# Kernel optimization log

Measured on AMD Instinct MI355X. Metric: run time of the kernel, lower is better.

## Reference

```python
import jax, jax.numpy as jnp
import numpy as np

DIM_Q = 512
DIM_K = 512
DIM_V = 512
NUM_HEADS = 8
B, NQ, NK = 4, 2048, 2048


def _linear_init(key, d_in, d_out):
    kw, kb = jax.random.split(key)
    bound = 1.0 / np.sqrt(d_in)
    W = jax.random.uniform(kw, (d_in, d_out), minval=-bound, maxval=bound, dtype=jnp.float32)
    b = jax.random.uniform(kb, (d_out,), minval=-bound, maxval=bound, dtype=jnp.float32)
    return W, b


def setup_inputs() -> dict:
    key = jax.random.key(0)
    ks = jax.random.split(key, 6)
    Q = jax.random.normal(ks[0], (B, NQ, DIM_Q), dtype=jnp.float32)
    K = jax.random.normal(ks[1], (B, NK, DIM_K), dtype=jnp.float32)
    Wq, bq = _linear_init(ks[2], DIM_Q, DIM_V)
    Wk, bk = _linear_init(ks[3], DIM_K, DIM_V)
    Wv, bv = _linear_init(ks[4], DIM_K, DIM_V)
    Wo, bo = _linear_init(ks[5], DIM_V, DIM_V)
    ln0_g = jnp.ones((DIM_V,), jnp.float32)
    ln0_b = jnp.zeros((DIM_V,), jnp.float32)
    ln1_g = jnp.ones((DIM_V,), jnp.float32)
    ln1_b = jnp.zeros((DIM_V,), jnp.float32)
    return {"Q": Q, "K": K, "Wq": Wq, "bq": bq, "Wk": Wk, "bk": bk,
            "Wv": Wv, "bv": bv, "Wo": Wo, "bo": bo,
            "ln0_g": ln0_g, "ln0_b": ln0_b, "ln1_g": ln1_g, "ln1_b": ln1_b}


def _layer_norm(x, g, b, eps=1e-5):
    mu = jnp.mean(x, axis=-1, keepdims=True)
    var = jnp.mean(jnp.square(x - mu), axis=-1, keepdims=True)
    return (x - mu) * jax.lax.rsqrt(var + eps) * g + b


def reference(Q, K, Wq, bq, Wk, bk, Wv, bv, Wo, bo, ln0_g, ln0_b, ln1_g, ln1_b):
    h = NUM_HEADS
    dh = DIM_V // h
    q = Q @ Wq + bq                      # [B, NQ, DIM_V]
    k = K @ Wk + bk                      # [B, NK, DIM_V]
    v = K @ Wv + bv                      # [B, NK, DIM_V]
    qh = q.reshape(B, NQ, h, dh)
    kh = k.reshape(B, NK, h, dh)
    vh = v.reshape(B, NK, h, dh)
    # NOTE: faithful to original — scale by sqrt(dim_V), not sqrt(head_dim)
    scores = jnp.einsum('bqhd,bkhd->bhqk', qh, kh) / jnp.sqrt(jnp.float32(DIM_V))
    A = jax.nn.softmax(scores, axis=-1)  # [B, h, NQ, NK]
    o = jnp.einsum('bhqk,bkhd->bqhd', A, vh) + qh
    H = o.reshape(B, NQ, DIM_V)          # residual with projected Q
    H = _layer_norm(H, ln0_g, ln0_b)
    H = H + jax.nn.relu(H @ Wo + bo)
    H = _layer_norm(H, ln1_g, ln1_b)
    return H
```

## Files before the change

kernel.cpp:

```cpp
#include <hip/hip_runtime.h>

typedef float f32x4 __attribute__((ext_vector_type(4)));
typedef __bf16 bf16x8 __attribute__((ext_vector_type(8)));
typedef unsigned short u16;
typedef u16 u16x8 __attribute__((ext_vector_type(8)));
typedef u16 u16x4 __attribute__((ext_vector_type(4)));

#define SCALE2F (0.044194173824159216f * 1.4426950408889634f)
#define UNSCALE (1.0f / SCALE2F)

__device__ __forceinline__ u16 f2bf(float x){ return __builtin_bit_cast(u16, (__bf16)x); }
__device__ __forceinline__ float bf2f(u16 h){ unsigned u = ((unsigned)h) << 16; return __builtin_bit_cast(float, u); }
__device__ __forceinline__ int swz(int r, int byteInRow){ return (r*128 + byteInRow) ^ ((r & 7) << 4); }
__device__ __forceinline__ void gload16(const void* g, void* l) {
  __builtin_amdgcn_global_load_lds(
      (const __attribute__((address_space(1))) void*)g,
      (__attribute__((address_space(3))) void*)l, 16, 0, 0);
}

#define MFMA(a,b,c) __builtin_amdgcn_mfma_f32_16x16x32_bf16((a),(b),(c),0,0,0)

__global__ __launch_bounds__(256) void wprep_k(
    const float* __restrict__ W0, const float* __restrict__ W1,
    const float* __restrict__ W2, const float* __restrict__ W3,
    u16* __restrict__ wt)
{
  __shared__ float tile[64][68];
  const float* Ws[4] = {W0, W1, W2, W3};
  const float* W = Ws[blockIdx.z];
  const float sc = (blockIdx.z == 0) ? SCALE2F : 1.0f;
  u16* out = wt + (size_t)blockIdx.z * 512 * 512;
  int k0 = blockIdx.x * 64, n0 = blockIdx.y * 64;
  int t = threadIdx.x;
  #pragma unroll
  for (int i = 0; i < 2; ++i) {
    int c = t + i*256; int r = c >> 3, k8 = c & 7;
    const float* src = W + (size_t)(k0 + r)*512 + n0 + k8*8;
    *(f32x4*)&tile[r][k8*8]     = *(const f32x4*)src;
    *(f32x4*)&tile[r][k8*8 + 4] = *(const f32x4*)(src + 4);
  }
  __syncthreads();
  #pragma unroll
  for (int i = 0; i < 2; ++i) {
    int c = t + i*256; int r = c >> 3, k8 = c & 7;
    u16x8 h;
    #pragma unroll
    for (int j = 0; j < 8; ++j) h[j] = f2bf(tile[k8*8 + j][r] * sc);
    *(u16x8*)(out + (size_t)(n0 + r)*512 + k0 + k8*8) = h;
  }
}

__global__ __launch_bounds__(512) void proj3_k(
    const float* __restrict__ Qin, const float* __restrict__ Kin,
    const u16* __restrict__ wt,
    const float* __restrict__ bq, const float* __restrict__ bk, const float* __restrict__ bv,
    u16* __restrict__ qbuf, u16* __restrict__ kbuf, u16* __restrict__ vt)
{
  __shared__ __align__(16) u16 lA[2][64*64];
  __shared__ __align__(16) u16 lB[2][128*64];
  int z = blockIdx.z;
  const float* A    = (z == 0) ? Qin : Kin;
  const u16*   Bt   = wt + (size_t)z * 262144;
  const float* bias = (z == 0) ? bq : (z == 1) ? bk : bv;
  const float bscale = (z == 0) ? SCALE2F : 1.0f;
  int row0 = blockIdx.x * 64, col0 = blockIdx.y * 128;
  int t = threadIdx.x, lane = t & 63, wid = t >> 6;
  int wr = wid >> 2, wc = wid & 3;
  int l15 = lane & 15, lg = lane >> 4;
  int ar = t >> 3, ak8 = t & 7;
  int br = t >> 3;
  int bsrc = (((t & 7) << 4) ^ ((br & 7) << 4)) >> 1;
  const float* Arow = A + (size_t)row0 * 512;
  const u16*   Brow = Bt + (size_t)col0 * 512;

  f32x4 acc[2][2] = {};

  #pragma unroll
  for (int i = 0; i < 2; ++i)
    gload16(Brow + (size_t)(br + i*64)*512 + bsrc, (char*)lB[0] + i*8192 + t*16);
  {
    const float* src = Arow + (size_t)ar*512 + ak8*8;
    f32x4 x0 = *(const f32x4*)src;
    f32x4 x1 = *(const f32x4*)(src + 4);
    u16x8 h;
    #pragma unroll
    for (int j = 0; j < 4; ++j) { h[j] = f2bf(x0[j]); h[j+4] = f2bf(x1[j]); }
    *(u16x8*)((char*)lA[0] + swz(ar, ak8*16)) = h;
  }
  __syncthreads();

  int cur = 0;
  for (int k0 = 0; k0 < 512; k0 += 64) {
    bool pf = (k0 + 64 < 512);
    f32x4 px0, px1;
    if (pf) {
      #pragma unroll
      for (int i = 0; i < 2; ++i)
        gload16(Brow + (size_t)(br + i*64)*512 + k0 + 64 + bsrc, (char*)lB[cur^1] + i*8192 + t*16);
      const float* src = Arow + (size_t)ar*512 + k0 + 64 + ak8*8;
      px0 = *(const f32x4*)src;
      px1 = *(const f32x4*)(src + 4);
    }
    const char* lAc = (const char*)lA[cur];
    const char* lBc = (const char*)lB[cur];
    #pragma unroll
    for (int ks = 0; ks < 2; ++ks) {
      bf16x8 af[2], bfv[2];
      #pragma unroll
      for (int m = 0; m < 2; ++m)
        af[m] = *(const bf16x8*)(lAc + swz(wr*32 + m*16 + l15, ks*64 + lg*16));
      #pragma unroll
      for (int n = 0; n < 2; ++n)
        bfv[n] = *(const bf16x8*)(lBc + swz(wc*32 + n*16 + l15, ks*64 + lg*16));
      #pragma unroll
      for (int m = 0; m < 2; ++m)
        #pragma unroll
        for (int n = 0; n < 2; ++n)
          acc[m][n] = MFMA(af[m], bfv[n], acc[m][n]);
    }
    if (pf) {
      u16x8 h;
      #pragma unroll
      for (int j = 0; j < 4; ++j) { h[j] = f2bf(px0[j]); h[j+4] = f2bf(px1[j]); }
      *(u16x8*)((char*)lA[cur^1] + swz(ar, ak8*16)) = h;
    }
    __syncthreads();
    cur ^= 1;
  }

  if (z < 2) {
    u16* out = z ? kbuf : qbuf;
    #pragma unroll
    for (int m = 0; m < 2; ++m) {
      int rowg = row0 + wr*32 + m*16 + lg*4;
      #pragma unroll
      for (int n = 0; n < 2; ++n) {
        int colg = col0 + wc*32 + n*16 + l15;
        float bvv = bias[colg] * bscale;
        #pragma unroll
        for (int r = 0; r < 4; ++r)
          out[(size_t)(rowg + r)*512 + colg] = f2bf(acc[m][n][r] + bvv);
      }
    }
  } else {
    #pragma unroll
    for (int m = 0; m < 2; ++m) {
      int rowg = row0 + wr*32 + m*16 + lg*4;
      int b = rowg >> 11, ntok = rowg & 2047;
      #pragma unroll
      for (int n = 0; n < 2; ++n) {
        int colg = col0 + wc*32 + n*16 + l15;
        float bvv = bias[colg];
        u16x4 hv;
        #pragma unroll
        for (int r = 0; r < 4; ++r) hv[r] = f2bf(acc[m][n][r] + bvv);
        *(u16x4*)(vt + ((size_t)b*512 + colg)*2048 + ntok) = hv;
      }
    }
  }
}

__global__ __launch_bounds__(512) void gemmo_k(
    const u16* __restrict__ A, const u16* __restrict__ Bt,
    const float* __restrict__ bias, float* __restrict__ outf,
    const u16* __restrict__ resid)
{
  __shared__ __align__(16) u16 lA[2][64*64];
  __shared__ __align__(16) u16 lB[2][128*64];
  int row0 = blockIdx.x * 64, col0 = blockIdx.y * 128;
  int t = threadIdx.x, lane = t & 63, wid = t >> 6;
  int wr = wid >> 2, wc = wid & 3;
  int l15 = lane & 15, lg = lane >> 4;
  int ar = t >> 3;
  int asrc = (((t & 7) << 4) ^ ((ar & 7) << 4)) >> 1;
  const u16* Arow = A + (size_t)row0 * 512;
  const u16* Brow = Bt + (size_t)col0 * 512;
  f32x4 acc[2][2] = {};

  gload16(Arow + (size_t)ar*512 + asrc, (char*)lA[0] + t*16);
  #pragma unroll
  for (int i = 0; i < 2; ++i)
    gload16(Brow + (size_t)(ar + i*64)*512 + asrc, (char*)lB[0] + i*8192 + t*16);
  __syncthreads();

  int cur = 0;
  for (int k0 = 0; k0 < 512; k0 += 64) {
    if (k0 + 64 < 512) {
      gload16(Arow + (size_t)ar*512 + k0 + 64 + asrc, (char*)lA[cur^1] + t*16);
      #pragma unroll
      for (int i = 0; i < 2; ++i)
        gload16(Brow + (size_t)(ar + i*64)*512 + k0 + 64 + asrc, (char*)lB[cur^1] + i*8192 + t*16);
    }
    const char* lAc = (const char*)lA[cur];
    const char* lBc = (const char*)lB[cur];
    #pragma unroll
    for (int ks = 0; ks < 2; ++ks) {
      bf16x8 af[2], bfv[2];
      #pragma unroll
      for (int m = 0; m < 2; ++m)
        af[m] = *(const bf16x8*)(lAc + swz(wr*32 + m*16 + l15, ks*64 + lg*16));
      #pragma unroll
      for (int n = 0; n < 2; ++n)
        bfv[n] = *(const bf16x8*)(lBc + swz(wc*32 + n*16 + l15, ks*64 + lg*16));
      #pragma unroll
      for (int m = 0; m < 2; ++m)
        #pragma unroll
        for (int n = 0; n < 2; ++n)
          acc[m][n] = MFMA(af[m], bfv[n], acc[m][n]);
    }
    __syncthreads();
    cur ^= 1;
  }
  #pragma unroll
  for (int m = 0; m < 2; ++m) {
    int rowg = row0 + wr*32 + m*16 + lg*4;
    #pragma unroll
    for (int n = 0; n < 2; ++n) {
      int colg = col0 + wc*32 + n*16 + l15;
      float bvv = bias[colg];
      #pragma unroll
      for (int r = 0; r < 4; ++r) {
        size_t idx = (size_t)(rowg + r)*512 + colg;
        outf[idx] = bf2f(resid[idx]) + fmaxf(acc[m][n][r] + bvv, 0.0f);
      }
    }
  }
}

__global__ __launch_bounds__(512) void attn_k(
    const u16* __restrict__ qb, const u16* __restrict__ kb,
    const u16* __restrict__ vt, float* __restrict__ opart, float* __restrict__ psb)
{
  __shared__ __align__(16) u16 lK[2][64*64];
  __shared__ __align__(16) u16 lV[2][64*64];
  __shared__ __align__(16) u16 pl[8][16][72];

  int t = threadIdx.x, lane = t & 63, wid = t >> 6;
  int bh = blockIdx.y;
  int b = bh >> 3, h = bh & 7;
  int zkv = blockIdx.z;
  int kvbeg = zkv * 1024, kvend = kvbeg + 1024;
  int q0 = blockIdx.x * 128 + wid * 16;
  int l15 = lane & 15, lg = lane >> 4;

  const u16* kbase = kb + ((size_t)b*2048)*512 + h*64;
  const u16* vbase = vt + ((size_t)b*512 + h*64)*2048;

  int sr = t >> 3;
  int ssrc = (((t & 7) << 4) ^ ((sr & 7) << 4)) >> 1;

  bf16x8 aq[2];
  {
    const u16* qp = qb + ((size_t)(b*2048 + q0 + l15))*512 + h*64 + lg*8;
    aq[0] = *(const bf16x8*)qp;
    aq[1] = *(const bf16x8*)(qp + 32);
  }

  f32x4 acco[4] = {};
  float ps = 0.0f;

  gload16(kbase + (size_t)(kvbeg + sr)*512 + ssrc, (char*)lK[0] + t*16);
  gload16(vbase + (size_t)sr*2048 + kvbeg + ssrc, (char*)lV[0] + t*16);
  __syncthreads();

  int cur = 0;
  for (int t0 = kvbeg; t0 < kvend; t0 += 64) {
    if (t0 + 64 < kvend) {
      gload16(kbase + (size_t)(t0 + 64 + sr)*512 + ssrc, (char*)lK[cur^1] + t*16);
      gload16(vbase + (size_t)sr*2048 + t0 + 64 + ssrc, (char*)lV[cur^1] + t*16);
    }
    f32x4 s[4] = {};
    const char* lKc = (const char*)lK[cur];
    #pragma unroll
    for (int n = 0; n < 4; ++n) {
      int row = n*16 + l15;
      bf16x8 bk0 = *(const bf16x8*)(lKc + swz(row, lg*16));
      bf16x8 bk1 = *(const bf16x8*)(lKc + swz(row, 64 + lg*16));
      s[n] = MFMA(bk0, aq[0], s[n]);
      s[n] = MFMA(bk1, aq[1], s[n]);
    }
    #pragma unroll
    for (int n = 0; n < 4; ++n) {
      u16x4 hp;
      #pragma unroll
      for (int r = 0; r < 4; ++r) {
        float p = __builtin_amdgcn_exp2f(s[n][r]);
        ps += p;
        hp[r] = f2bf(p);
      }
      *(u16x4*)&pl[wid][l15][n*16 + lg*4] = hp;
    }
    const char* lVc = (const char*)lV[cur];
    #pragma unroll
    for (int ks = 0; ks < 2; ++ks) {
      bf16x8 pb = *(const bf16x8*)&pl[wid][l15][ks*32 + lg*8];
      #pragma unroll
      for (int n = 0; n < 4; ++n) {
        bf16x8 av = *(const bf16x8*)(lVc + swz(n*16 + l15, ks*64 + lg*16));
        acco[n] = MFMA(av, pb, acco[n]);
      }
    }
    __syncthreads();
    cur ^= 1;
  }
  ps += __shfl_xor(ps, 16, 64);
  ps += __shfl_xor(ps, 32, 64);
  float* obase = opart + (((size_t)zkv*4 + b)*2048 + q0 + l15)*512 + h*64;
  #pragma unroll
  for (int n = 0; n < 4; ++n)
    *(f32x4*)(obase + n*16 + lg*4) = acco[n];
  if (lg == 0)
    psb[((size_t)zkv*32 + bh)*2048 + q0 + l15] = ps;
}

__global__ __launch_bounds__(256) void ln0c_k(
    const float* __restrict__ opart, const float* __restrict__ psb,
    const u16* __restrict__ qb, const float* __restrict__ gam,
    const float* __restrict__ bet, u16* __restrict__ yh)
{
  int t = threadIdx.x, lane = t & 63, w = t >> 6;
  size_t row = (size_t)blockIdx.x * 4 + w;
  int b = (int)(row >> 11), q = (int)(row & 2047);
  int head = lane >> 3;
  float sa = psb[((size_t)b*8 + head)*2048 + q] +
             psb[((size_t)32 + b*8 + head)*2048 + q];
  float inv = 1.0f / sa;
  const float* xa = opart + row*512 + lane*8;
  const float* xb = xa + (size_t)8192*512;
  f32x4 a0 = *(const f32x4*)xa,      a1 = *(const f32x4*)(xa + 4);
  f32x4 b0v = *(const f32x4*)xb,     b1v = *(const f32x4*)(xb + 4);
  u16x8 qr = *(const u16x8*)(qb + row*512 + lane*8);
  f32x4 v0, v1;
  #pragma unroll
  for (int j = 0; j < 4; ++j) {
    v0[j] = (a0[j] + b0v[j])*inv + bf2f(qr[j])*UNSCALE;
    v1[j] = (a1[j] + b1v[j])*inv + bf2f(qr[j+4])*UNSCALE;
  }
  float s = 0.0f, ss = 0.0f;
  #pragma unroll
  for (int j = 0; j < 4; ++j) {
    s += v0[j] + v1[j];
    ss += v0[j]*v0[j] + v1[j]*v1[j];
  }
  #pragma unroll
  for (int m = 1; m < 64; m <<= 1) { s += __shfl_xor(s, m, 64); ss += __shfl_xor(ss, m, 64); }
  float mu = s * (1.0f/512.0f);
  float var = ss * (1.0f/512.0f) - mu*mu;
  float rs = rsqrtf(var + 1e-5f);
  const float* gp = gam + lane*8;
  const float* bp = bet + lane*8;
  f32x4 g0 = *(const f32x4*)gp, g1 = *(const f32x4*)(gp + 4);
  f32x4 be0 = *(const f32x4*)bp, be1 = *(const f32x4*)(bp + 4);
  u16x8 hv;
  #pragma unroll
  for (int j = 0; j < 4; ++j) {
    hv[j]   = f2bf((v0[j] - mu)*rs*g0[j] + be0[j]);
    hv[j+4] = f2bf((v1[j] - mu)*rs*g1[j] + be1[j]);
  }
  *(u16x8*)(yh + row*512 + lane*8) = hv;
}

__global__ __launch_bounds__(256) void ln_k(
    const float* __restrict__ x, const float* __restrict__ gam,
    const float* __restrict__ bet, float* __restrict__ y)
{
  int t = threadIdx.x, lane = t & 63, w = t >> 6;
  size_t row = (size_t)blockIdx.x * 4 + w;
  const float* xp = x + row*512 + lane*8;
  f32x4 v0 = *(const f32x4*)xp;
  f32x4 v1 = *(const f32x4*)(xp + 4);
  float s = 0.0f, ss = 0.0f;
  #pragma unroll
  for (int j = 0; j < 4; ++j) {
    s += v0[j] + v1[j];
    ss += v0[j]*v0[j] + v1[j]*v1[j];
  }
  #pragma unroll
  for (int m = 1; m < 64; m <<= 1) { s += __shfl_xor(s, m, 64); ss += __shfl_xor(ss, m, 64); }
  float mu = s * (1.0f/512.0f);
  float var = ss * (1.0f/512.0f) - mu*mu;
  float rs = rsqrtf(var + 1e-5f);
  const float* gp = gam + lane*8;
  const float* bp = bet + lane*8;
  f32x4 g0 = *(const f32x4*)gp, g1 = *(const f32x4*)(gp + 4);
  f32x4 b0 = *(const f32x4*)bp, b1 = *(const f32x4*)(bp + 4);
  f32x4 o0, o1;
  #pragma unroll
  for (int j = 0; j < 4; ++j) {
    o0[j] = (v0[j] - mu)*rs*g0[j] + b0[j];
    o1[j] = (v1[j] - mu)*rs*g1[j] + b1[j];
  }
  float* yp = y + row*512 + lane*8;
  *(f32x4*)yp = o0;
  *(f32x4*)(yp + 4) = o1;
}

extern "C" void kernel_launch(void* const* d_in, const int* in_sizes, int n_in,
                              void* d_out, int out_size, void* d_ws, size_t ws_size,
                              hipStream_t stream)
{
  const float* Q   = (const float*)d_in[0];
  const float* K   = (const float*)d_in[1];
  const float* Wq  = (const float*)d_in[2];
  const float* bq  = (const float*)d_in[3];
  const float* Wk  = (const float*)d_in[4];
  const float* bk  = (const float*)d_in[5];
  const float* Wv  = (const float*)d_in[6];
  const float* bv  = (const float*)d_in[7];
  const float* Wo  = (const float*)d_in[8];
  const float* bo  = (const float*)d_in[9];
  const float* g0  = (const float*)d_in[10];
  const float* b0  = (const float*)d_in[11];
  const float* g1  = (const float*)d_in[12];
  const float* b1  = (const float*)d_in[13];

  char* ws = (char*)d_ws;
  u16*   wt    = (u16*)(ws + 0);
  u16*   qbuf  = (u16*)(ws + (2u<<20));
  u16*   kbuf  = (u16*)(ws + (10u<<20));
  u16*   vt    = (u16*)(ws + (18u<<20));
  float* opart = (float*)(ws + (26u<<20));
  float* psb   = (float*)(ws + (58u<<20));
  u16*   Hbuf  = (u16*)(ws + (10u<<20));
  float* Gbuf  = (float*)(ws + (26u<<20));

  wprep_k<<<dim3(8, 8, 4), 256, 0, stream>>>(Wq, Wk, Wv, Wo, wt);
  proj3_k<<<dim3(128, 4, 3), 512, 0, stream>>>(Q, K, wt, bq, bk, bv, qbuf, kbuf, vt);
  attn_k<<<dim3(16, 32, 2), 512, 0, stream>>>(qbuf, kbuf, vt, opart, psb);
  ln0c_k<<<2048, 256, 0, stream>>>(opart, psb, qbuf, g0, b0, Hbuf);
  gemmo_k<<<dim3(128, 4), 512, 0, stream>>>(Hbuf, wt + 3*262144, bo, Gbuf, Hbuf);
  ln_k<<<2048, 256, 0, stream>>>(Gbuf, g1, b1, (float*)d_out);
}
```

Before: 113.6 us.

## Use 32x32x16 MFMA in attention with 32 query rows per wave

The attention kernel moves from 16x16x32 to 32x32x16 bf16 MFMA, so each wave handles 32 query rows instead of 16 and each block covers 256 queries, halving the grid in x. Each K/V tile loaded into LDS is therefore reused across twice as many queries, cutting K/V global and LDS traffic per query and the number of MFMA instructions issued. The cost is more accumulator registers (two 16-float accumulators plus a 16-float score tile) and a larger per-wave P staging buffer. The grid falls to 512 blocks, which may underfill the GPU, and launch_bounds now requests 4 blocks per CU.

```diff
diff --git a/kernel.cpp b/kernel.cpp
--- a/kernel.cpp
+++ b/kernel.cpp
@@ -1,6 +1,7 @@
 #include <hip/hip_runtime.h>
 
 typedef float f32x4 __attribute__((ext_vector_type(4)));
+typedef float f32x16 __attribute__((ext_vector_type(16)));
 typedef __bf16 bf16x8 __attribute__((ext_vector_type(8)));
 typedef unsigned short u16;
 typedef u16 u16x8 __attribute__((ext_vector_type(8)));
@@ -18,7 +19,8 @@
       (__attribute__((address_space(3))) void*)l, 16, 0, 0);
 }
 
-#define MFMA(a,b,c) __builtin_amdgcn_mfma_f32_16x16x32_bf16((a),(b),(c),0,0,0)
+#define MFMA(a,b,c)   __builtin_amdgcn_mfma_f32_16x16x32_bf16((a),(b),(c),0,0,0)
+#define MFMA32(a,b,c) __builtin_amdgcn_mfma_f32_32x32x16_bf16((a),(b),(c),0,0,0)
 
 __global__ __launch_bounds__(256) void wprep_k(
     const float* __restrict__ W0, const float* __restrict__ W1,
@@ -227,21 +229,21 @@
   }
 }
 
-__global__ __launch_bounds__(512) void attn_k(
+__global__ __launch_bounds__(512, 4) void attn_k(
     const u16* __restrict__ qb, const u16* __restrict__ kb,
     const u16* __restrict__ vt, float* __restrict__ opart, float* __restrict__ psb)
 {
   __shared__ __align__(16) u16 lK[2][64*64];
   __shared__ __align__(16) u16 lV[2][64*64];
-  __shared__ __align__(16) u16 pl[8][16][72];
+  __shared__ __align__(16) u16 pl[8][32][72];
 
   int t = threadIdx.x, lane = t & 63, wid = t >> 6;
   int bh = blockIdx.y;
   int b = bh >> 3, h = bh & 7;
   int zkv = blockIdx.z;
   int kvbeg = zkv * 1024, kvend = kvbeg + 1024;
-  int q0 = blockIdx.x * 128 + wid * 16;
-  int l15 = lane & 15, lg = lane >> 4;
+  int q0 = blockIdx.x * 256 + wid * 32;
+  int l31 = lane & 31, hi = lane >> 5;
 
   const u16* kbase = kb + ((size_t)b*2048)*512 + h*64;
   const u16* vbase = vt + ((size_t)b*512 + h*64)*2048;
@@ -249,14 +251,14 @@
   int sr = t >> 3;
   int ssrc = (((t & 7) << 4) ^ ((sr & 7) << 4)) >> 1;
 
-  bf16x8 aq[2];
+  bf16x8 aq[4];
   {
-    const u16* qp = qb + ((size_t)(b*2048 + q0 + l15))*512 + h*64 + lg*8;
-    aq[0] = *(const bf16x8*)qp;
-    aq[1] = *(const bf16x8*)(qp + 32);
-  }
-
-  f32x4 acco[4] = {};
+    const u16* qp = qb + ((size_t)(b*2048 + q0 + l31))*512 + h*64 + hi*8;
+    #pragma unroll
+    for (int ks = 0; ks < 4; ++ks) aq[ks] = *(const bf16x8*)(qp + ks*16);
+  }
+
+  f32x16 acco[2] = {};
   float ps = 0.0f;
 
   gload16(kbase + (size_t)(kvbeg + sr)*512 + ssrc, (char*)lK[0] + t*16);
@@ -269,48 +271,55 @@
       gload16(kbase + (size_t)(t0 + 64 + sr)*512 + ssrc, (char*)lK[cur^1] + t*16);
       gload16(vbase + (size_t)sr*2048 + t0 + 64 + ssrc, (char*)lV[cur^1] + t*16);
     }
-    f32x4 s[4] = {};
     const char* lKc = (const char*)lK[cur];
-    #pragma unroll
-    for (int n = 0; n < 4; ++n) {
-      int row = n*16 + l15;
-      bf16x8 bk0 = *(const bf16x8*)(lKc + swz(row, lg*16));
-      bf16x8 bk1 = *(const bf16x8*)(lKc + swz(row, 64 + lg*16));
-      s[n] = MFMA(bk0, aq[0], s[n]);
-      s[n] = MFMA(bk1, aq[1], s[n]);
-    }
-    #pragma unroll
-    for (int n = 0; n < 4; ++n) {
-      u16x4 hp;
-      #pragma unroll
-      for (int r = 0; r < 4; ++r) {
-        float p = __builtin_amdgcn_exp2f(s[n][r]);
-        ps += p;
-        hp[r] = f2bf(p);
-      }
-      *(u16x4*)&pl[wid][l15][n*16 + lg*4] = hp;
-    }
     const char* lVc = (const char*)lV[cur];
     #pragma unroll
-    for (int ks = 0; ks < 2; ++ks) {
-      bf16x8 pb = *(const bf16x8*)&pl[wid][l15][ks*32 + lg*8];
-      #pragma unroll
-      for (int n = 0; n < 4; ++n) {
-        bf16x8 av = *(const bf16x8*)(lVc + swz(n*16 + l15, ks*64 + lg*16));
-        acco[n] = MFMA(av, pb, acco[n]);
-      }
-    }
+    for (int n = 0; n < 2; ++n) {
+      f32x16 s = {};
+      #pragma unroll
+      for (int ks = 0; ks < 4; ++ks) {
+        bf16x8 kf = *(const bf16x8*)(lKc + swz(n*32 + l31, ks*32 + hi*16));
+        s = MFMA32(kf, aq[ks], s);
+      }
+      #pragma unroll
+      for (int rq = 0; rq < 4; ++rq) {
+        u16x4 hp;
+        #pragma unroll
+        for (int e = 0; e < 4; ++e) {
+          float p = __builtin_amdgcn_exp2f(s[rq*4 + e]);
+          ps += p;
+          hp[e] = f2bf(p);
+        }
+        *(u16x4*)&pl[wid][l31][n*32 + rq*8 + hi*4] = hp;
+      }
+    }
+    bf16x8 pf[4];
+    #pragma unroll
+    for (int ks = 0; ks < 4; ++ks)
+      pf[ks] = *(const bf16x8*)&pl[wid][l31][ks*16 + hi*8];
+    #pragma unroll
+    for (int m = 0; m < 2; ++m)
+      #pragma unroll
+      for (int ks = 0; ks < 4; ++ks) {
+        bf16x8 vf = *(const bf16x8*)(lVc + swz(m*32 + l31, ks*32 + hi*16));
+        acco[m] = MFMA32(vf, pf[ks], acco[m]);
+      }
     __syncthreads();
     cur ^= 1;
   }
-  ps += __shfl_xor(ps, 16, 64);
   ps += __shfl_xor(ps, 32, 64);
-  float* obase = opart + (((size_t)zkv*4 + b)*2048 + q0 + l15)*512 + h*64;
-  #pragma unroll
-  for (int n = 0; n < 4; ++n)
-    *(f32x4*)(obase + n*16 + lg*4) = acco[n];
-  if (lg == 0)
-    psb[((size_t)zkv*32 + bh)*2048 + q0 + l15] = ps;
+  float* obase = opart + (((size_t)zkv*4 + b)*2048 + q0 + l31)*512 + h*64;
+  #pragma unroll
+  for (int m = 0; m < 2; ++m)
+    #pragma unroll
+    for (int rq = 0; rq < 4; ++rq) {
+      f32x4 ov;
+      #pragma unroll
+      for (int e = 0; e < 4; ++e) ov[e] = acco[m][rq*4 + e];
+      *(f32x4*)(obase + m*32 + rq*8 + hi*4) = ov;
+    }
+  if (hi == 0)
+    psb[((size_t)zkv*32 + bh)*2048 + q0 + l31] = ps;
 }
 
 __global__ __launch_bounds__(256) void ln0c_k(
@@ -426,7 +435,7 @@
 
   wprep_k<<<dim3(8, 8, 4), 256, 0, stream>>>(Wq, Wk, Wv, Wo, wt);
   proj3_k<<<dim3(128, 4, 3), 512, 0, stream>>>(Q, K, wt, bq, bk, bv, qbuf, kbuf, vt);
-  attn_k<<<dim3(16, 32, 2), 512, 0, stream>>>(qbuf, kbuf, vt, opart, psb);
+  attn_k<<<dim3(8, 32, 2), 512, 0, stream>>>(qbuf, kbuf, vt, opart, psb);
   ln0c_k<<<2048, 256, 0, stream>>>(opart, psb, qbuf, g0, b0, Hbuf);
   gemmo_k<<<dim3(128, 4), 512, 0, stream>>>(Hbuf, wt + 3*262144, bo, Gbuf, Hbuf);
   ln_k<<<2048, 256, 0, stream>>>(Gbuf, g1, b1, (float*)d_out);
```

Measured after the change: 105.6 us. -7.1%, faster.
